# Performance work log

Hardware: AMD Instinct MI355X
Metric: run time of the kernel (lower is better)

## Reference

```python
import jax, jax.numpy as jnp
import numpy as np

FILTER_ORDER = 49   # M
FRAME_PERIOD = 80   # P
IGNORE_GAIN = False


def linear_interpolation(b, P):
    """Upsample frame-level coeffs (..., N, D) -> (..., N*P, D).

    Matches diffsptk LinearInterpolation: replicate-pad last frame, then
    linear interpolation with align_corners=True, i.e.
    h[n*P + p] = (1 - p/P) * b[n] + (p/P) * b[min(n+1, N-1)].
    """
    if P == 1:
        return b
    N, D = b.shape[-2], b.shape[-1]
    left = b                                             # (..., N, D)
    right = jnp.concatenate([b[..., 1:, :], b[..., -1:, :]], axis=-2)  # (..., N, D)
    w = (jnp.arange(P, dtype=b.dtype) / P)[:, None]      # (P, 1)
    h = left[..., :, None, :] * (1 - w) + right[..., :, None, :] * w  # (..., N, P, D)
    return h.reshape(*b.shape[:-2], N * P, D)


def setup_inputs() -> dict:
    key = jax.random.key(0)
    k1, k2 = jax.random.split(key)
    B = 8
    N = 3000                       # number of frames
    T = N * FRAME_PERIOD           # 240000 samples
    x = jax.random.normal(k1, (B, T), dtype=jnp.float32)
    b = jax.random.normal(k2, (B, N, FILTER_ORDER + 1), dtype=jnp.float32)
    return {"x": x, "b": b}


def reference(x, b):
    M = b.shape[-1] - 1
    T = x.shape[-1]
    # per-sample filter taps, flipped so h[..., k] multiplies x[t - M + k]
    h = linear_interpolation(jnp.flip(b, axis=-1), FRAME_PERIOD)  # (B, T, M+1)
    if IGNORE_GAIN:
        h = h / h[..., -1:]
    xp = jnp.pad(x, ((0, 0), (M, 0)))                    # (B, T+M)
    idx = jnp.arange(T)[:, None] + jnp.arange(M + 1)[None, :]  # (T, M+1)
    windows = xp[:, idx]                                 # (B, T, M+1)
    y = jnp.sum(windows * h, axis=-1)                    # (B, T)
    return y
```

## Files before the change

kernel.cpp:

```cpp
#include <hip/hip_runtime.h>

constexpr int TAPS    = 50;
constexpr int P       = 80;
constexpr int BLOCK   = 256;
constexpr int R       = 4;
constexpr int WFR     = 5;
constexpr int FSTRIDE = 52;
constexpr int WAVES   = BLOCK / 64;
constexpr int XWIN    = 56;

__global__ __launch_bounds__(BLOCK) void azdf_kernel(
    const float* __restrict__ x, const float* __restrict__ b,
    float* __restrict__ y, int T, int N) {
  __shared__ float bs[WAVES * WFR * FSTRIDE];

  const int batch = blockIdx.y;
  const int tid   = threadIdx.x;
  const int wave  = __builtin_amdgcn_readfirstlane(tid >> 6);
  const int lane  = tid & 63;
  const float* xb = x + (size_t)batch * T;
  const float* bb = b + (size_t)batch * N * TAPS;

  const int w0      = (blockIdx.x * BLOCK + wave * 64) * R;
  const int n_first = w0 / P;
  float* wbs = &bs[wave * WFR * FSTRIDE];

  const int t_base = w0 + lane * R;
  const bool active = (t_base < T);

  float xr[XWIN];
  if (active) {
    if (t_base >= 52) {
      const float* xp = xb + t_base - 52;
#pragma unroll
      for (int j = 0; j < XWIN / 4; ++j) {
        float4 v = *(const float4*)(xp + 4 * j);
        xr[4*j+0] = v.x; xr[4*j+1] = v.y; xr[4*j+2] = v.z; xr[4*j+3] = v.w;
      }
    } else {
#pragma unroll
      for (int i = 0; i < XWIN; ++i) {
        int xi = t_base - 52 + i;
        xr[i] = (xi >= 0) ? xb[xi] : 0.0f;
      }
    }
  }

  if (lane < TAPS / 2) {
#pragma unroll
    for (int f = 0; f < WFR; ++f) {
      int n = n_first + f;
      if (n > N - 1) n = N - 1;
      *(float2*)&wbs[f * FSTRIDE + 2 * lane] =
          *(const float2*)&bb[(size_t)n * TAPS + 2 * lane];
    }
  }

  if (!active) return;

  const int n = t_base / P;
  const float* c0 = &wbs[(n - n_first) * FSTRIDE];
  const float* c1 = c0 + FSTRIDE;

  float s0[R], s1[R];
#pragma unroll
  for (int r = 0; r < R; ++r) { s0[r] = 0.0f; s1[r] = 0.0f; }

#pragma unroll
  for (int kc = 0; kc < 48; kc += 4) {
    float4 a0 = *(const float4*)&c0[kc];
    float4 a1 = *(const float4*)&c1[kc];
    const float av0[4] = {a0.x, a0.y, a0.z, a0.w};
    const float av1[4] = {a1.x, a1.y, a1.z, a1.w};
#pragma unroll
    for (int kk = 0; kk < 4; ++kk) {
      const int k = kc + kk;
#pragma unroll
      for (int r = 0; r < R; ++r) {
        float xv = xr[52 + r - k];
        s0[r] = fmaf(xv, av0[kk], s0[r]);
        s1[r] = fmaf(xv, av1[kk], s1[r]);
      }
    }
  }
  {
    float2 a0 = *(const float2*)&c0[48];
    float2 a1 = *(const float2*)&c1[48];
#pragma unroll
    for (int r = 0; r < R; ++r) {
      float xv = xr[52 + r - 48];
      s0[r] = fmaf(xv, a0.x, s0[r]);
      s1[r] = fmaf(xv, a1.x, s1[r]);
    }
#pragma unroll
    for (int r = 0; r < R; ++r) {
      float xv = xr[52 + r - 49];
      s0[r] = fmaf(xv, a0.y, s0[r]);
      s1[r] = fmaf(xv, a1.y, s1[r]);
    }
  }

  const int phase = t_base - n * P;
  float out[R];
#pragma unroll
  for (int r = 0; r < R; ++r) {
    float w = (float)(phase + r) * (1.0f / (float)P);
    out[r] = (1.0f - w) * s0[r] + w * s1[r];
  }

  float* yp = y + (size_t)batch * T + t_base;
  *(float4*)yp = make_float4(out[0], out[1], out[2], out[3]);
}

extern "C" void kernel_launch(void* const* d_in, const int* in_sizes, int n_in,
                              void* d_out, int out_size, void* d_ws, size_t ws_size,
                              hipStream_t stream) {
  const float* x = (const float*)d_in[0];
  const float* b = (const float*)d_in[1];
  float* y = (float*)d_out;

  const int B = 8;
  const int N = in_sizes[1] / (B * TAPS);
  const int T = N * P;

  const int threads_per_batch = T / R;
  dim3 grid((threads_per_batch + BLOCK - 1) / BLOCK, B);
  azdf_kernel<<<grid, BLOCK, 0, stream>>>(x, b, y, T, N);
}
```

Measured before the change: 74.49 us.

## Double outputs per thread and stage input window cooperatively in swizzled LDS

Each thread now computes 8 consecutive outputs instead of 4, so every coefficient read from LDS is reused across more samples. Each wave now loads its whole input window, including the 52-sample halo, into an XOR-swizzled LDS region using coalesced float4 loads. Lanes then read their 60-float register window back from LDS instead of each fetching overlapping global data. In exchange, register pressure rises, each wave needs more LDS, and correctness depends on ordering LDS accesses within a wave, since there is no barrier.

```diff
diff --git a/kernel.cpp b/kernel.cpp
--- a/kernel.cpp
+++ b/kernel.cpp
@@ -3,63 +3,82 @@
 constexpr int TAPS    = 50;
 constexpr int P       = 80;
 constexpr int BLOCK   = 256;
-constexpr int R       = 4;
-constexpr int WFR     = 5;
+constexpr int R       = 8;
+constexpr int WFR     = 9;
 constexpr int FSTRIDE = 52;
 constexpr int WAVES   = BLOCK / 64;
-constexpr int XWIN    = 56;
+constexpr int WOUT    = 64 * R;
+constexpr int XWF     = WOUT + 52;
+constexpr int XWC     = XWF / 4;
+constexpr int XBUF    = 576;
+constexpr int CBUF    = WFR * FSTRIDE;
+constexpr int WLDS    = XBUF + CBUF;
 
 __global__ __launch_bounds__(BLOCK) void azdf_kernel(
     const float* __restrict__ x, const float* __restrict__ b,
     float* __restrict__ y, int T, int N) {
-  __shared__ float bs[WAVES * WFR * FSTRIDE];
+  __shared__ __align__(16) float bs[WAVES * WLDS];
 
   const int batch = blockIdx.y;
   const int tid   = threadIdx.x;
-  const int wave  = __builtin_amdgcn_readfirstlane(tid >> 6);
+  const int wave  = tid >> 6;
   const int lane  = tid & 63;
   const float* xb = x + (size_t)batch * T;
   const float* bb = b + (size_t)batch * N * TAPS;
 
-  const int w0      = (blockIdx.x * BLOCK + wave * 64) * R;
-  const int n_first = w0 / P;
-  float* wbs = &bs[wave * WFR * FSTRIDE];
+  const int w0 = (blockIdx.x * BLOCK + wave * 64) * R;
+  if (w0 >= T) return;
 
-  const int t_base = w0 + lane * R;
-  const bool active = (t_base < T);
+  float* xw  = &bs[wave * WLDS];
+  float* wcs = xw + XBUF;
 
-  float xr[XWIN];
-  if (active) {
-    if (t_base >= 52) {
-      const float* xp = xb + t_base - 52;
+  const bool edge = (w0 == 0) || (w0 + WOUT > T);
+  if (!edge) {
+    const float* xp = xb + (w0 - 52);
 #pragma unroll
-      for (int j = 0; j < XWIN / 4; ++j) {
-        float4 v = *(const float4*)(xp + 4 * j);
-        xr[4*j+0] = v.x; xr[4*j+1] = v.y; xr[4*j+2] = v.z; xr[4*j+3] = v.w;
+    for (int rd = 0; rd < 3; ++rd) {
+      int c = lane + rd * 64;
+      if (c < XWC) {
+        float4 v = *(const float4*)(xp + 4 * c);
+        int cs = c ^ ((c >> 3) & 7);
+        *(float4*)&xw[4 * cs] = v;
       }
-    } else {
-#pragma unroll
-      for (int i = 0; i < XWIN; ++i) {
-        int xi = t_base - 52 + i;
-        xr[i] = (xi >= 0) ? xb[xi] : 0.0f;
-      }
+    }
+  } else {
+    for (int i = lane; i < XWF; i += 64) {
+      int xi = w0 - 52 + i;
+      float v = (xi >= 0 && xi < T) ? xb[xi] : 0.0f;
+      int c  = i >> 2;
+      int cs = c ^ ((c >> 3) & 7);
+      xw[4 * cs + (i & 3)] = v;
     }
   }
 
+  const int n_first = w0 / P;
   if (lane < TAPS / 2) {
 #pragma unroll
     for (int f = 0; f < WFR; ++f) {
       int n = n_first + f;
       if (n > N - 1) n = N - 1;
-      *(float2*)&wbs[f * FSTRIDE + 2 * lane] =
+      *(float2*)&wcs[f * FSTRIDE + 2 * lane] =
           *(const float2*)&bb[(size_t)n * TAPS + 2 * lane];
     }
   }
 
-  if (!active) return;
+  const int t_base = w0 + lane * R;
+  if (t_base >= T) return;
+
+  float xr[60];
+#pragma unroll
+  for (int j = 0; j < 15; ++j) {
+    int c  = 2 * lane + j;
+    int cs = c ^ ((c >> 3) & 7);
+    float4 v = *(const float4*)&xw[4 * cs];
+    xr[4*j+0] = v.x; xr[4*j+1] = v.y; xr[4*j+2] = v.z; xr[4*j+3] = v.w;
+  }
 
   const int n = t_base / P;
-  const float* c0 = &wbs[(n - n_first) * FSTRIDE];
+  const float* c0 = &wcs[(n - n_first) * FSTRIDE];
   const float* c1 = c0 + FSTRIDE;
 
   float s0[R], s1[R];
@@ -109,7 +128,8 @@
   }
 
   float* yp = y + (size_t)batch * T + t_base;
-  *(float4*)yp = make_float4(out[0], out[1], out[2], out[3]);
+  *(float4*)(yp + 0) = make_float4(out[0], out[1], out[2], out[3]);
+  *(float4*)(yp + 4) = make_float4(out[4], out[5], out[6], out[7]);
 }
 
 extern "C" void kernel_launch(void* const* d_in, const int* in_sizes, int n_in,
```

Result: faster. 69.51 us (-6.7%).
